# Performance work log

Hardware: AMD Instinct MI355X
Metric: run time of the kernel (lower is better)

Reference implementation:

```python
import jax, jax.numpy as jnp
import numpy as np

B, S, D, K = 8, 2048, 256, 8192
BETA = 0.25


def setup_inputs() -> dict:
    key = jax.random.key(0)
    k0, k1, k2, k3 = jax.random.split(key, 4)
    scale = 1.0 / np.sqrt(D).astype(np.float32)
    return {
        "x": jax.random.normal(k0, (B, S, D), jnp.float32),
        "embedding": jax.random.normal(k1, (K, D), jnp.float32),
        "W1": jax.random.normal(k2, (D, D), jnp.float32) * scale,
        "b1": jnp.zeros((D,), jnp.float32),
        "W2": jax.random.normal(k3, (D, D), jnp.float32) * scale,
        "b2": jnp.zeros((D,), jnp.float32),
    }


def reference(x, embedding, W1, b1, W2, b2):
    d = x.shape[-1]
    x_flat = x.reshape(-1, d)  # [N, D]
    # squared euclidean distance to every codebook vector: [N, K]
    dist = (
        jnp.sum(embedding * embedding, axis=1)[None, :]
        - 2.0 * jnp.einsum("nd,kd->nk", x_flat, embedding)
        + jnp.sum(x_flat * x_flat, axis=1, keepdims=True)
    )
    idx = jnp.argmin(dist, axis=1)                               # [N]
    min_dist = jnp.take_along_axis(dist, idx[:, None], axis=1)[:, 0]  # [N]
    z = embedding[idx].reshape(x.shape)                          # gather + reshape
    # implicit neural codebook: residual MLP correction
    r = x - z
    h = jax.nn.relu(jnp.einsum("bsd,de->bse", r, W1) + b1)
    z = z + jnp.einsum("bsd,de->bse", h, W2) + b2
    loss = BETA * jnp.mean(min_dist)
    return z, loss
```

## Files before the change

### kernel.cpp

```cpp
#include <hip/hip_runtime.h>
#include <cfloat>

#define N_TOK 16384
#define DIM 256
#define KCB 8192
#define BETA_C 0.25f
#define NSPLIT 8
#define NCHUNK 32
#define MARGIN 4.0f

typedef __attribute__((ext_vector_type(8))) short short8;
typedef __attribute__((ext_vector_type(4))) float f32x4;
typedef unsigned short ushort_t;

__device__ __forceinline__ void async_copy16(const void* g, void* l) {
    __builtin_amdgcn_global_load_lds(
        (const __attribute__((address_space(1))) unsigned int*)g,
        (__attribute__((address_space(3))) unsigned int*)l, 16, 0, 0);
}

__device__ __forceinline__ void merge2(float& v1, int& i1, float& v2, int& i2,
                                       float b1, int j1, float b2, int j2) {
    const bool bf_ = (b1 < v1) || (b1 == v1 && j1 < i1);
    const float nv1 = bf_ ? b1 : v1; const int ni1 = bf_ ? j1 : i1;
    const float c = bf_ ? v1 : b1;   const int ci = bf_ ? i1 : j1;
    const float d = bf_ ? b2 : v2;   const int di = bf_ ? j2 : i2;
    const bool ds_ = (d < c) || (d == c && di < ci);
    v1 = nv1; i1 = ni1;
    v2 = ds_ ? d : c; i2 = ds_ ? di : ci;
}

template <int WITH_NORM>
__global__ void __launch_bounds__(256)
prep1_kernel(const float* __restrict__ src, ushort_t* __restrict__ dst,
             float* __restrict__ norm, int nrows) {
    const int w = threadIdx.x >> 6, lane = threadIdx.x & 63;
    const int r = blockIdx.x * 4 + w;
    if (r >= nrows) return;
    const float4 v = *reinterpret_cast<const float4*>(src + (size_t)r * DIM + lane * 4);
    const unsigned u0 = __float_as_uint(v.x), u1 = __float_as_uint(v.y);
    const unsigned u2 = __float_as_uint(v.z), u3 = __float_as_uint(v.w);
    *reinterpret_cast<uint2*>(dst + (size_t)r * DIM + lane * 4) =
        make_uint2((u0 >> 16) | (u1 & 0xFFFF0000u), (u2 >> 16) | (u3 & 0xFFFF0000u));
    if (WITH_NORM) {
        float s = v.x * v.x + v.y * v.y + v.z * v.z + v.w * v.w;
#pragma unroll
        for (int o = 32; o > 0; o >>= 1) s += __shfl_down(s, o, 64);
        if (lane == 0) norm[r] = s;
    }
}

__global__ void wt_kernel(const float* __restrict__ W, ushort_t* __restrict__ WT) {
    const int flat = blockIdx.x * 256 + threadIdx.x;
    const int d = flat >> 8, e = flat & 255;
    WT[(size_t)e * 256 + d] = (ushort_t)(__float_as_uint(W[flat]) >> 16);
}

__global__ void __launch_bounds__(256, 2)
dist_kernel(const ushort_t* __restrict__ X2, const ushort_t* __restrict__ E2,
            const float* __restrict__ enorm, uint4* __restrict__ mg) {
    __shared__ char sb[65536];
    __shared__ float enormS[1024];

    const int tid = threadIdx.x;
    const int lane = tid & 63;
    const int w = tid >> 6;
    const int wy = w >> 1, wx = w & 1;
    const int l15 = lane & 15, l4 = lane >> 4;
    const int row0 = blockIdx.x * 128;
    const int col_base = blockIdx.y * 1024;
    const int rr = lane >> 3;
    const int egr = (lane & 7) ^ rr;

#pragma unroll
    for (int i = 0; i < 4; ++i) enormS[tid + 256 * i] = enorm[col_base + tid + 256 * i];

    float tv1[16], tv2[16];
    int ti1[16], ti2[16];
#pragma unroll
    for (int s = 0; s < 16; ++s) { tv1[s] = FLT_MAX; tv2[s] = FLT_MAX; ti1[s] = 0; ti2[s] = 0; }

    f32x4 acc[4][4];

#define STAGE_CHUNK(buf, c)                                                        \
    {                                                                              \
        const int kt_ = (c) >> 2, dq_ = (c) & 3;                                   \
        const int off_ = dq_ * 64;                                                 \
        const ushort_t* Ab_ = X2 + (size_t)row0 * DIM + off_ + egr * 8;            \
        const ushort_t* Bb_ = E2 + (size_t)(col_base + kt_ * 128) * DIM + off_ + egr * 8; \
        char* Al_ = sb + (buf) * 16384;                                            \
        char* Bl_ = sb + 32768 + (buf) * 16384;                                    \
        _Pragma("unroll")                                                          \
        for (int i_ = 0; i_ < 4; ++i_) {                                           \
            const int g_ = w * 4 + i_;                                             \
            async_copy16(Ab_ + (size_t)(g_ * 8 + rr) * DIM, Al_ + g_ * 1024);      \
            async_copy16(Bb_ + (size_t)(g_ * 8 + rr) * DIM, Bl_ + g_ * 1024);      \
        }                                                                          \
    }

    STAGE_CHUNK(0, 0)
    __syncthreads();

    for (int c = 0; c < NCHUNK; ++c) {
        const int cur = c & 1;
        const int cp = c & 3;
        if (c + 1 < NCHUNK) STAGE_CHUNK(cur ^ 1, c + 1)

        if (cp == 0) {
#pragma unroll
            for (int m = 0; m < 4; ++m)
#pragma unroll
                for (int n = 0; n < 4; ++n) {
                    f32x4 z = {0.f, 0.f, 0.f, 0.f};
                    acc[m][n] = z;
                }
        }

        const char* Al = sb + cur * 16384;
        const char* Bl = sb + 32768 + cur * 16384;
#pragma unroll
        for (int ks = 0; ks < 2; ++ks) {
            short8 af[4], bf[4];
#pragma unroll
            for (int m = 0; m < 4; ++m) {
                const int r = wy * 64 + m * 16 + l15;
                af[m] = *reinterpret_cast<const short8*>(
                    Al + r * 128 + ((ks * 64 + l4 * 16) ^ ((r & 7) << 4)));
            }
#pragma unroll
            for (int n = 0; n < 4; ++n) {
                const int r = wx * 64 + n * 16 + l15;
                bf[n] = *reinterpret_cast<const short8*>(
                    Bl + r * 128 + ((ks * 64 + l4 * 16) ^ ((r & 7) << 4)));
            }
#pragma unroll
            for (int m = 0; m < 4; ++m)
#pragma unroll
                for (int n = 0; n < 4; ++n)
                    acc[m][n] = __builtin_amdgcn_mfma_f32_16x16x32_bf16(af[m], bf[n], acc[m][n], 0, 0, 0);
        }

        if (cp == 3) {
            const int klocal = (c >> 2) * 128;
#pragma unroll
            for (int n = 0; n < 4; ++n) {
                const int cl = klocal + wx * 64 + n * 16 + l15;
                const float en = enormS[cl];
                const int kg = col_base + cl;
#pragma unroll
                for (int m = 0; m < 4; ++m)
#pragma unroll
                    for (int j = 0; j < 4; ++j) {
                        const float v = fmaf(-2.f, acc[m][n][j], en);
                        const int s = m * 4 + j;
                        const bool c1 = v < tv1[s];
                        const bool c2 = v < tv2[s];
                        tv2[s] = c1 ? tv1[s] : (c2 ? v : tv2[s]);
                        ti2[s] = c1 ? ti1[s] : (c2 ? kg : ti2[s]);
                        tv1[s] = c1 ? v : tv1[s];
                        ti1[s] = c1 ? kg : ti1[s];
                    }
            }
        }
        __syncthreads();
    }

    uint4* sc = reinterpret_cast<uint4*>(sb);
#pragma unroll
    for (int s = 0; s < 16; ++s)
        sc[tid + 256 * s] = make_uint4(__float_as_uint(tv1[s]), (unsigned)ti1[s],
                                       __float_as_uint(tv2[s]), (unsigned)ti2[s]);
    __syncthreads();
    if (tid < 128) {
        const int r = tid;
        const int wy2 = r >> 6, lr = r & 63;
        const int m = lr >> 4, g = (lr & 15) >> 2, j = lr & 3, s = m * 4 + j;
        float v1 = FLT_MAX, v2 = FLT_MAX;
        int i1 = 0, i2 = 0;
        for (int wx2 = 0; wx2 < 2; ++wx2)
            for (int c = 0; c < 16; ++c) {
                const int thr = (wy2 * 2 + wx2) * 64 + g * 16 + c;
                const uint4 q = sc[thr + 256 * s];
                const float a1 = __uint_as_float(q.x), a2 = __uint_as_float(q.z);
                if (a1 < v1) {
                    if (a2 < v1) { v1 = a1; i1 = (int)q.y; v2 = a2; i2 = (int)q.w; }
                    else { v2 = v1; i2 = i1; v1 = a1; i1 = (int)q.y; }
                } else if (a1 < v2) { v2 = a1; i2 = (int)q.y; }
            }
        mg[(size_t)(row0 + r) * NSPLIT + blockIdx.y] =
            make_uint4(__float_as_uint(v1), (unsigned)i1, __float_as_uint(v2), (unsigned)i2);
    }
}

__global__ void __launch_bounds__(256)
merge_fixup_kernel(const float* __restrict__ x, const float* __restrict__ emb,
                   const uint4* __restrict__ mg, int* __restrict__ idx_out,
                   float* __restrict__ minq) {
    const int w = threadIdx.x >> 6, lane = threadIdx.x & 63;
    const int n = blockIdx.x * 4 + w;
    const uint4 q = mg[(size_t)n * NSPLIT + (lane & 7)];
    const float v = (lane < 32) ? __uint_as_float(q.x) : __uint_as_float(q.z);
    const int ki = (lane < 32) ? (int)q.y : (int)q.w;

    float m = v;
#pragma unroll
    for (int o = 1; o < 64; o <<= 1) m = fminf(m, __shfl_xor(m, o, 64));

    const unsigned long long mask = __ballot(v <= m + MARGIN && (lane & 31) < NSPLIT);
    const float4 xv = *reinterpret_cast<const float4*>(x + (size_t)n * DIM + lane * 4);

    float bestv = FLT_MAX;
    int bestk = 0x7fffffff;
    unsigned long long mm = mask;
    while (mm) {
        const int src = __ffsll((long long)mm) - 1;
        mm &= mm - 1;
        const int k = __shfl(ki, src, 64);
        const float4 ev = *reinterpret_cast<const float4*>(emb + (size_t)k * DIM + lane * 4);
        const float dx = xv.x - ev.x, dy = xv.y - ev.y, dz = xv.z - ev.z, dw = xv.w - ev.w;
        float s = dx * dx + dy * dy + dz * dz + dw * dw;
#pragma unroll
        for (int o = 32; o > 0; o >>= 1) s += __shfl_xor(s, o, 64);
        if (s < bestv || (s == bestv && k < bestk)) { bestv = s; bestk = k; }
    }
    if (lane == 0) {
        idx_out[n] = bestk;
        minq[n] = bestv;
    }
}

__global__ void __launch_bounds__(256)
fused_mlp_kernel(const float* __restrict__ x, const float* __restrict__ emb,
                 const int* __restrict__ idx, const ushort_t* __restrict__ W1T,
                 const ushort_t* __restrict__ W2T, const float* __restrict__ b1,
                 const float* __restrict__ b2, float* __restrict__ z) {
    __shared__ char sb[65536];
    __shared__ int idxs[64];

    const int tid = threadIdx.x;
    const int lane = tid & 63;
    const int w = tid >> 6;
    const int l15 = lane & 15, l4 = lane >> 4;
    const int rr = lane >> 3;
    const int egr = (lane & 7) ^ rr;
    const int row0 = blockIdx.x * 64;

    if (tid < 64) idxs[tid] = idx[row0 + tid];
    __syncthreads();

#pragma unroll
    for (int j = 0; j < 16; ++j) {
        const int flat = tid + 256 * j;
        const int r = flat >> 6;
        const int sg = flat & 63;
        const float4 xv = *reinterpret_cast<const float4*>(x + (size_t)(row0 + r) * DIM + sg * 4);
        const float4 ev = *reinterpret_cast<const float4*>(emb + (size_t)idxs[r] * DIM + sg * 4);
        const unsigned u0 = __float_as_uint(xv.x - ev.x), u1 = __float_as_uint(xv.y - ev.y);
        const unsigned u2 = __float_as_uint(xv.z - ev.z), u3 = __float_as_uint(xv.w - ev.w);
        const uint2 pk = make_uint2((u0 >> 16) | (u1 & 0xFFFF0000u),
                                    (u2 >> 16) | (u3 & 0xFFFF0000u));
        *reinterpret_cast<uint2*>(sb + r * 512 + ((sg * 8) ^ ((r & 7) << 4))) = pk;
    }

    const ushort_t* Wp[2] = {W1T, W2T};
    f32x4 acc[4][4];

    for (int layer = 0; layer < 2; ++layer) {
        const ushort_t* WT = Wp[layer];
#pragma unroll
        for (int m = 0; m < 4; ++m)
#pragma unroll
            for (int n = 0; n < 4; ++n) {
                f32x4 zz = {0.f, 0.f, 0.f, 0.f};
                acc[m][n] = zz;
            }
        for (int kc = 0; kc < 4; ++kc) {
            __syncthreads();
#pragma unroll
            for (int i = 0; i < 8; ++i) {
                const int g = w * 8 + i;
                async_copy16(WT + (size_t)(g * 8 + rr) * 256 + kc * 64 + egr * 8,
                             sb + 32768 + g * 1024);
            }
            __syncthreads();
#pragma unroll
            for (int ks = 0; ks < 2; ++ks) {
                short8 af[4], bf[4];
#pragma unroll
                for (int m = 0; m < 4; ++m) {
                    const int r = m * 16 + l15;
                    af[m] = *reinterpret_cast<const short8*>(
                        sb + r * 512 + ((((kc * 2 + ks) * 64) + l4 * 16) ^ ((r & 7) << 4)));
                }
#pragma unroll
                for (int n = 0; n < 4; ++n) {
                    const int r = w * 64 + n * 16 + l15;
                    bf[n] = *reinterpret_cast<const short8*>(
                        sb + 32768 + r * 128 + ((ks * 64 + l4 * 16) ^ ((r & 7) << 4)));
                }
#pragma unroll
                for (int m = 0; m < 4; ++m)
#pragma unroll
                    for (int n = 0; n < 4; ++n)
                        acc[m][n] = __builtin_amdgcn_mfma_f32_16x16x32_bf16(af[m], bf[n], acc[m][n], 0, 0, 0);
            }
        }

        if (layer == 0) {
            float b1v[4];
#pragma unroll
            for (int n = 0; n < 4; ++n) b1v[n] = b1[w * 64 + n * 16 + l15];
            __syncthreads();
#pragma unroll
            for (int m = 0; m < 4; ++m)
#pragma unroll
                for (int n = 0; n < 4; ++n)
#pragma unroll
                    for (int j = 0; j < 4; ++j) {
                        const int row = m * 16 + l4 * 4 + j;
                        const int col = w * 64 + n * 16 + l15;
                        const float hv = fmaxf(acc[m][n][j] + b1v[n], 0.f);
                        *reinterpret_cast<ushort_t*>(
                            sb + row * 512 + ((col * 2) ^ ((row & 7) << 4))) =
                            (ushort_t)(__float_as_uint(hv) >> 16);
                    }
            __syncthreads();
        } else {
            float b2v[4];
#pragma unroll
            for (int n = 0; n < 4; ++n) b2v[n] = b2[w * 64 + n * 16 + l15];
#pragma unroll
            for (int m = 0; m < 4; ++m)
#pragma unroll
                for (int n = 0; n < 4; ++n)
#pragma unroll
                    for (int j = 0; j < 4; ++j) {
                        const int row = m * 16 + l4 * 4 + j;
                        const int col = w * 64 + n * 16 + l15;
                        const float ev = emb[(size_t)idxs[row] * DIM + col];
                        z[(size_t)(row0 + row) * DIM + col] = acc[m][n][j] + b2v[n] + ev;
                    }
        }
    }
}

__global__ void loss_kernel(const float* __restrict__ minq, float* __restrict__ loss_out) {
    const int tid = threadIdx.x;
    float s = 0.f;
    for (int i = tid; i < N_TOK; i += 256) s += minq[i];
#pragma unroll
    for (int o = 32; o > 0; o >>= 1) s += __shfl_down(s, o, 64);
    __shared__ float sbf[4];
    if ((tid & 63) == 0) sbf[tid >> 6] = s;
    __syncthreads();
    if (tid == 0) loss_out[0] = BETA_C * ((sbf[0] + sbf[1] + sbf[2] + sbf[3]) / (float)N_TOK);
}

extern "C" void kernel_launch(void* const* d_in, const int* in_sizes, int n_in,
                              void* d_out, int out_size, void* d_ws, size_t ws_size,
                              hipStream_t stream) {
    const float* x   = (const float*)d_in[0];
    const float* emb = (const float*)d_in[1];
    const float* W1  = (const float*)d_in[2];
    const float* b1  = (const float*)d_in[3];
    const float* W2  = (const float*)d_in[4];
    const float* b2  = (const float*)d_in[5];

    float* z_out = (float*)d_out;
    float* loss_out = z_out + (size_t)N_TOK * DIM;

    char* ws = (char*)d_ws;
    float*    enorm = (float*)(ws);
    int*      idxb  = (int*)(ws + 32768);
    float*    minq  = (float*)(ws + 98304);
    ushort_t* W1T   = (ushort_t*)(ws + 163840);
    ushort_t* W2T   = (ushort_t*)(ws + 294912);
    ushort_t* E2    = (ushort_t*)(ws + 425984);
    ushort_t* X2    = (ushort_t*)(ws + 4620288);
    uint4*    mg    = (uint4*)(ws + 13008896);

    hipLaunchKernelGGL((prep1_kernel<1>), dim3(KCB / 4), dim3(256), 0, stream,
                       emb, E2, enorm, KCB);
    hipLaunchKernelGGL((prep1_kernel<0>), dim3(N_TOK / 4), dim3(256), 0, stream,
                       x, X2, (float*)nullptr, N_TOK);
    hipLaunchKernelGGL(wt_kernel, dim3(256), dim3(256), 0, stream, W1, W1T);
    hipLaunchKernelGGL(wt_kernel, dim3(256), dim3(256), 0, stream, W2, W2T);
    hipLaunchKernelGGL(dist_kernel, dim3(N_TOK / 128, NSPLIT), dim3(256), 0, stream,
                       X2, E2, enorm, mg);
    hipLaunchKernelGGL(merge_fixup_kernel, dim3(N_TOK / 4), dim3(256), 0, stream,
                       x, emb, mg, idxb, minq);
    hipLaunchKernelGGL(fused_mlp_kernel, dim3(N_TOK / 64), dim3(256), 0, stream,
                       x, emb, idxb, W1T, W2T, b1, b2, z_out);
    hipLaunchKernelGGL(loss_kernel, dim3(1), dim3(256), 0, stream, minq, loss_out);
}
```

Before: 170.0 us.

## Single-buffer dist kernel LDS for higher occupancy and shuffle-based top-2 reduction

Drops the double-buffered async LDS staging in the distance GEMM kernel and uses one 32KB buffer, loading each chunk and then synchronizing. Launch bounds go from 2 to 4 blocks per CU so more waves can hide latency in place of software pipelining. The final per-row top-2 merge now uses wavefront shuffles plus a small LDS exchange, replacing a 256x16 LDS dump and a serial scan. This gives up load/compute overlap within a block and may cause register spilling under the tighter launch bound.

```diff
diff --git a/kernel.cpp b/kernel.cpp
--- a/kernel.cpp
+++ b/kernel.cpp
@@ -56,10 +56,10 @@
     WT[(size_t)e * 256 + d] = (ushort_t)(__float_as_uint(W[flat]) >> 16);
 }
 
-__global__ void __launch_bounds__(256, 2)
+__global__ void __launch_bounds__(256, 4)
 dist_kernel(const ushort_t* __restrict__ X2, const ushort_t* __restrict__ E2,
             const float* __restrict__ enorm, uint4* __restrict__ mg) {
-    __shared__ char sb[65536];
+    __shared__ char sb[32768];
     __shared__ float enormS[1024];
 
     const int tid = threadIdx.x;
@@ -82,29 +82,24 @@
 
     f32x4 acc[4][4];
 
-#define STAGE_CHUNK(buf, c)                                                        \
+#define STAGE_CHUNK(c)                                                             \
     {                                                                              \
         const int kt_ = (c) >> 2, dq_ = (c) & 3;                                   \
         const int off_ = dq_ * 64;                                                 \
         const ushort_t* Ab_ = X2 + (size_t)row0 * DIM + off_ + egr * 8;            \
         const ushort_t* Bb_ = E2 + (size_t)(col_base + kt_ * 128) * DIM + off_ + egr * 8; \
-        char* Al_ = sb + (buf) * 16384;                                            \
-        char* Bl_ = sb + 32768 + (buf) * 16384;                                    \
         _Pragma("unroll")                                                          \
         for (int i_ = 0; i_ < 4; ++i_) {                                           \
             const int g_ = w * 4 + i_;                                             \
-            async_copy16(Ab_ + (size_t)(g_ * 8 + rr) * DIM, Al_ + g_ * 1024);      \
-            async_copy16(Bb_ + (size_t)(g_ * 8 + rr) * DIM, Bl_ + g_ * 1024);      \
+            async_copy16(Ab_ + (size_t)(g_ * 8 + rr) * DIM, sb + g_ * 1024);       \
+            async_copy16(Bb_ + (size_t)(g_ * 8 + rr) * DIM, sb + 16384 + g_ * 1024); \
         }                                                                          \
     }
 
-    STAGE_CHUNK(0, 0)
-    __syncthreads();
-
     for (int c = 0; c < NCHUNK; ++c) {
-        const int cur = c & 1;
         const int cp = c & 3;
-        if (c + 1 < NCHUNK) STAGE_CHUNK(cur ^ 1, c + 1)
+        STAGE_CHUNK(c)
+        __syncthreads();
 
         if (cp == 0) {
 #pragma unroll
@@ -116,8 +111,6 @@
                 }
         }
 
-        const char* Al = sb + cur * 16384;
-        const char* Bl = sb + 32768 + cur * 16384;
 #pragma unroll
         for (int ks = 0; ks < 2; ++ks) {
             short8 af[4], bf[4];
@@ -125,13 +118,13 @@
             for (int m = 0; m < 4; ++m) {
                 const int r = wy * 64 + m * 16 + l15;
                 af[m] = *reinterpret_cast<const short8*>(
-                    Al + r * 128 + ((ks * 64 + l4 * 16) ^ ((r & 7) << 4)));
+                    sb + r * 128 + ((ks * 64 + l4 * 16) ^ ((r & 7) << 4)));
             }
 #pragma unroll
             for (int n = 0; n < 4; ++n) {
                 const int r = wx * 64 + n * 16 + l15;
                 bf[n] = *reinterpret_cast<const short8*>(
-                    Bl + r * 128 + ((ks * 64 + l4 * 16) ^ ((r & 7) << 4)));
+                    sb + 16384 + r * 128 + ((ks * 64 + l4 * 16) ^ ((r & 7) << 4)));
             }
 #pragma unroll
             for (int m = 0; m < 4; ++m)
@@ -165,29 +158,34 @@
         __syncthreads();
     }
 
-    uint4* sc = reinterpret_cast<uint4*>(sb);
-#pragma unroll
-    for (int s = 0; s < 16; ++s)
-        sc[tid + 256 * s] = make_uint4(__float_as_uint(tv1[s]), (unsigned)ti1[s],
-                                       __float_as_uint(tv2[s]), (unsigned)ti2[s]);
+    uint4* sm2 = reinterpret_cast<uint4*>(sb);
+#pragma unroll
+    for (int s = 0; s < 16; ++s) {
+        float v1 = tv1[s], v2 = tv2[s];
+        int i1 = ti1[s], i2 = ti2[s];
+#pragma unroll
+        for (int o = 1; o < 16; o <<= 1) {
+            const float b1 = __shfl_xor(v1, o, 64), b2 = __shfl_xor(v2, o, 64);
+            const int j1 = __shfl_xor(i1, o, 64), j2 = __shfl_xor(i2, o, 64);
+            merge2(v1, i1, v2, i2, b1, j1, b2, j2);
+        }
+        if (l15 == 0) {
+            const int row = wy * 64 + (s >> 2) * 16 + l4 * 4 + (s & 3);
+            sm2[wx * 128 + row] = make_uint4(__float_as_uint(v1), (unsigned)i1,
+                                             __float_as_uint(v2), (unsigned)i2);
+        }
+    }
     __syncthreads();
     if (tid < 128) {
-        const int r = tid;
-        const int wy2 = r >> 6, lr = r & 63;
-        const int m = lr >> 4, g = (lr & 15) >> 2, j = lr & 3, s = m * 4 + j;
         float v1 = FLT_MAX, v2 = FLT_MAX;
-        int i1 = 0, i2 = 0;
-        for (int wx2 = 0; wx2 < 2; ++wx2)
-            for (int c = 0; c < 16; ++c) {
-                const int thr = (wy2 * 2 + wx2) * 64 + g * 16 + c;
-                const uint4 q = sc[thr + 256 * s];
-                const float a1 = __uint_as_float(q.x), a2 = __uint_as_float(q.z);
-                if (a1 < v1) {
-                    if (a2 < v1) { v1 = a1; i1 = (int)q.y; v2 = a2; i2 = (int)q.w; }
-                    else { v2 = v1; i2 = i1; v1 = a1; i1 = (int)q.y; }
-                } else if (a1 < v2) { v2 = a1; i2 = (int)q.y; }
-            }
-        mg[(size_t)(row0 + r) * NSPLIT + blockIdx.y] =
+        int i1 = 0x7fffffff, i2 = 0x7fffffff;
+#pragma unroll
+        for (int wx2 = 0; wx2 < 2; ++wx2) {
+            const uint4 q = sm2[wx2 * 128 + tid];
+            merge2(v1, i1, v2, i2, __uint_as_float(q.x), (int)q.y,
+                   __uint_as_float(q.z), (int)q.w);
+        }
+        mg[(size_t)(row0 + tid) * NSPLIT + blockIdx.y] =
             make_uint4(__float_as_uint(v1), (unsigned)i1, __float_as_uint(v2), (unsigned)i2);
     }
 }
```

Result: slower. 378.7 us (+122.7%).
